# Kernel optimization log

Measured on AMD Instinct MI355X. Metric: run time of the kernel, lower is better.

## Reference

```python
import jax, jax.numpy as jnp
import numpy as np

N_USERS = 100000
N_ITEMS = 50000
D = 64
E = 3200000
N_LAYERS = 2
ALPHA = 0.1


def setup_inputs() -> dict:
    key = jax.random.key(0)
    k1, k2, k3, k4 = jax.random.split(key, 4)
    user_emb0 = jax.random.normal(k1, (N_USERS, D), jnp.float32) * 0.01
    item_emb0 = jax.random.normal(k2, (N_ITEMS, D), jnp.float32) * 0.01
    edge_u = jax.random.randint(k3, (E,), 0, N_USERS, dtype=jnp.int32)
    edge_i = jax.random.randint(k4, (E,), 0, N_ITEMS, dtype=jnp.int32)
    ones = jnp.ones((E,), jnp.float32)
    # row-normalization exactly as the torch module: A_ui = D_u^{-1} R, A_iu = D_i^{-1} R^T
    deg_u = jax.ops.segment_sum(ones, edge_u, num_segments=N_USERS)
    deg_i = jax.ops.segment_sum(ones, edge_i, num_segments=N_ITEMS)
    deg_u = jnp.where(deg_u == 0, 1.0, deg_u)
    deg_i = jnp.where(deg_i == 0, 1.0, deg_i)
    a_ui_vals = 1.0 / deg_u[edge_u]  # value of A_ui at (u, i)
    a_iu_vals = 1.0 / deg_i[edge_i]  # value of A_iu at (i, u)
    return {
        "user_emb0": user_emb0,
        "item_emb0": item_emb0,
        "a_ui_vals": a_ui_vals,
        "a_iu_vals": a_iu_vals,
        "edge_u": edge_u,
        "edge_i": edge_i,
    }


def _spmm(vals, dst_idx, src_idx, src_emb, n_dst):
    # out[dst] = sum_e vals[e] * src_emb[src_idx[e]]  -- gather, scale, scatter-add
    gathered = src_emb[src_idx] * vals[:, None]  # [E, D]
    return jax.ops.segment_sum(gathered, dst_idx, num_segments=n_dst)


def reference(user_emb0, item_emb0, a_ui_vals, a_iu_vals, edge_u, edge_i):
    user_layers = [user_emb0]
    item_layers = [item_emb0]
    for _ in range(N_LAYERS):
        u_new = _spmm(a_ui_vals, edge_u, edge_i, item_layers[-1], N_USERS) + ALPHA * user_emb0
        i_new = _spmm(a_iu_vals, edge_i, edge_u, user_layers[-1], N_ITEMS) + ALPHA * item_emb0
        user_layers.append(u_new)
        item_layers.append(i_new)
    # [n_layers+1, N_USERS, D], [n_layers+1, N_ITEMS, D]
    return jnp.stack(user_layers, 0), jnp.stack(item_layers, 0)
```

## Files before the change

### kernel.cpp

```cpp
#include <hip/hip_runtime.h>


constexpr int N_USERS = 100000;
constexpr int N_ITEMS = 50000;
constexpr int N_ROWS  = N_USERS + N_ITEMS;
constexpr int D = 64;
constexpr int E_EDGES = 3200000;
constexpr float ALPHA = 0.1f;

constexpr long long NUF = (long long)N_USERS * D;
constexpr long long NIF = (long long)N_ITEMS * D;

constexpr int SB_SHIFT = 8;
constexpr int SB_ROWS  = 1 << SB_SHIFT;
constexpr int NSB      = (N_ROWS + SB_ROWS - 1) >> SB_SHIFT;
constexpr int CAP      = 20480;

constexpr int P1_EDGES   = 8192;
constexpr int P1_THREADS = 512;
constexpr int P1_EPT     = P1_EDGES / P1_THREADS;
constexpr int P2_THREADS = 512;

__global__ void init_layer0_sb(const float* __restrict__ uemb,
                               const float* __restrict__ iemb,
                               float* __restrict__ out,
                               int* __restrict__ sbcur) {
    if (blockIdx.x == 0) {
        for (int k = threadIdx.x; k < NSB; k += blockDim.x)
            sbcur[k] = k * CAP;
    }
    long long idx = (long long)blockIdx.x * blockDim.x + threadIdx.x;
    if (idx < NUF) out[idx] = uemb[idx];
    if (idx < NIF) out[3 * NUF + idx] = iemb[idx];
}

__global__ void init_layer0(const float* __restrict__ uemb,
                            const float* __restrict__ iemb,
                            float* __restrict__ out) {
    long long idx = (long long)blockIdx.x * blockDim.x + threadIdx.x;
    if (idx < NUF) out[idx] = uemb[idx];
    if (idx < NIF) out[3 * NUF + idx] = iemb[idx];
}

__global__ void seed_alpha(const float* __restrict__ uemb,
                           const float* __restrict__ iemb,
                           float* __restrict__ out) {
    long long idx = (long long)blockIdx.x * blockDim.x + threadIdx.x;
    if (idx < NUF) {
        float av = ALPHA * uemb[idx];
        out[NUF + idx] = av;
        out[2 * NUF + idx] = av;
    }
    if (idx < NIF) {
        float av = ALPHA * iemb[idx];
        out[3 * NUF + NIF + idx] = av;
        out[3 * NUF + 2 * NIF + idx] = av;
    }
}

__global__ void phase1_binsort(const int* __restrict__ eu, const int* __restrict__ ei,
                               int* __restrict__ sbcur, unsigned* __restrict__ scratch) {
    __shared__ int hist[NSB];
    __shared__ int gbase[NSB];
    int t = threadIdx.x;
    int nchunks = (E_EDGES + P1_EDGES - 1) / P1_EDGES;
    for (int c = blockIdx.x; c < nchunks; c += gridDim.x) {
        int lo = c * P1_EDGES;
        for (int r = t; r < NSB; r += P1_THREADS) hist[r] = 0;
        __syncthreads();
        unsigned sbr[2 * P1_EPT];
        unsigned val[2 * P1_EPT];
#pragma unroll
        for (int k = 0; k < P1_EPT; k++) {
            int e = lo + k * P1_THREADS + t;
            if (e < E_EDGES) {
                int u = __builtin_nontemporal_load(eu + e);
                int i = __builtin_nontemporal_load(ei + e);
                int r0 = u;
                int r1 = N_USERS + i;
                int sb0 = r0 >> SB_SHIFT;
                int sb1 = r1 >> SB_SHIFT;
                int rk0 = atomicAdd(&hist[sb0], 1);
                int rk1 = atomicAdd(&hist[sb1], 1);
                sbr[2 * k]     = ((unsigned)sb0 << 16) | (unsigned)rk0;
                val[2 * k]     = ((unsigned)(r0 & (SB_ROWS - 1)) << 17) | (unsigned)i;
                sbr[2 * k + 1] = ((unsigned)sb1 << 16) | (unsigned)rk1;
                val[2 * k + 1] = ((unsigned)(r1 & (SB_ROWS - 1)) << 17) | (unsigned)u;
            } else {
                sbr[2 * k]     = 0xFFFFFFFFu;
                sbr[2 * k + 1] = 0xFFFFFFFFu;
            }
        }
        __syncthreads();
        for (int r = t; r < NSB; r += P1_THREADS) {
            int cnt = hist[r];
            gbase[r] = cnt ? atomicAdd(&sbcur[r], cnt) : 0;
        }
        __syncthreads();
#pragma unroll
        for (int k = 0; k < 2 * P1_EPT; k++) {
            if (sbr[k] != 0xFFFFFFFFu) {
                int sb = (int)(sbr[k] >> 16);
                int rk = (int)(sbr[k] & 0xFFFFu);
                int p  = gbase[sb] + rk;
                if (p < (sb + 1) * CAP)
                    scratch[p] = val[k];
            }
        }
        __syncthreads();
    }
}

__global__ void phase2_fused(const unsigned* __restrict__ scratch,
                             const int* __restrict__ sbcur,
                             int* __restrict__ row, int* __restrict__ col) {
    __shared__ unsigned buf[CAP];
    __shared__ int hist[SB_ROWS];
    __shared__ int pscan[SB_ROWS];
    __shared__ int psc[P2_THREADS];
    __shared__ int exls[NSB + 1];
    int sb = blockIdx.x;
    int t = threadIdx.x;
    int a = (2 * t < NSB) ? (sbcur[2 * t] - (2 * t) * CAP) : 0;
    int b = (2 * t + 1 < NSB) ? (sbcur[2 * t + 1] - (2 * t + 1) * CAP) : 0;
    psc[t] = a + b;
    __syncthreads();
    for (int off = 1; off < P2_THREADS; off <<= 1) {
        int x = (t >= off) ? psc[t - off] : 0;
        __syncthreads();
        psc[t] += x;
        __syncthreads();
    }
    int base = psc[t] - (a + b);
    if (2 * t < NSB)     exls[2 * t] = base;
    if (2 * t + 1 < NSB) exls[2 * t + 1] = base + a;
    if (t < SB_ROWS) hist[t] = 0;
    __syncthreads();
    int lo = sb * CAP;
    int n  = sbcur[sb] - lo;
    if (n > CAP) n = CAP;
    int out_lo = exls[sb];
    for (int idx = t; idx < n; idx += P2_THREADS)
        atomicAdd(&hist[scratch[lo + idx] >> 17], 1);
    __syncthreads();
    if (t < SB_ROWS) pscan[t] = hist[t];
    __syncthreads();
    for (int off = 1; off < SB_ROWS; off <<= 1) {
        int x = 0;
        if (t < SB_ROWS && t >= off) x = pscan[t - off];
        __syncthreads();
        if (t < SB_ROWS) pscan[t] += x;
        __syncthreads();
    }
    int excl = 0;
    if (t < SB_ROWS) {
        excl = pscan[t] - hist[t];
        int gr = (sb << SB_SHIFT) + t;
        if (gr <= N_ROWS) row[gr] = out_lo + excl;
    }
    __syncthreads();
    if (t < SB_ROWS) hist[t] = excl;
    __syncthreads();
    for (int idx = t; idx < n; idx += P2_THREADS) {
        unsigned e = scratch[lo + idx];
        int p = atomicAdd(&hist[e >> 17], 1);
        buf[p] = e & 0x1FFFFu;
    }
    __syncthreads();
    for (int k = t; k < n; k += P2_THREADS)
        col[out_lo + k] = (int)buf[k];
}

__global__ void emb_to_int8(const float* __restrict__ uemb,
                            const float* __restrict__ iemb,
                            signed char* __restrict__ q0u,
                            signed char* __restrict__ q0i,
                            float* __restrict__ s0u,
                            float* __restrict__ s0i) {
    long long gtid = (long long)blockIdx.x * blockDim.x + threadIdx.x;
    int wave = (int)(gtid >> 6);
    int lane = (int)(gtid & 63);
    if (wave >= N_ROWS) return;
    const float* src; signed char* q; float* s; int r;
    if (wave < N_USERS) { r = wave; src = uemb; q = q0u; s = s0u; }
    else { r = wave - N_USERS; src = iemb; q = q0i; s = s0i; }
    long long li = ((long long)r << 6) + lane;
    float v = src[li];
    float av = fabsf(v);
#pragma unroll
    for (int off = 32; off > 0; off >>= 1)
        av = fmaxf(av, __shfl_xor(av, off));
    float sc = (av > 0.f) ? av / 127.f : 1.f;
    q[li] = (signed char)rintf(v / sc);
    if (lane == 0) s[r] = sc;
}

__device__ __forceinline__ void pull_row_q(const int* __restrict__ row,
                                           const int* __restrict__ col,
                                           const signed char* __restrict__ qsrc,
                                           const float* __restrict__ ssrc,
                                           const float* __restrict__ e0f,
                                           float* __restrict__ dst,
                                           signed char* __restrict__ qdst,
                                           float* __restrict__ sdst,
                                           int comb_row, int local_row, int lane) {
    int start = __builtin_amdgcn_readfirstlane(row[comb_row]);
    int end   = __builtin_amdgcn_readfirstlane(row[comb_row + 1]);
    int len = end - start;
    float scale = (len > 0) ? 1.0f / (float)len : 0.0f;

    float acc0 = 0.f, acc1 = 0.f, acc2 = 0.f, acc3 = 0.f;
    int j = start;
    for (; j + 16 <= end; j += 16) {
        int c[16];
#pragma unroll
        for (int k = 0; k < 16; k++)
            c[k] = __builtin_nontemporal_load(col + j + k);
        float g[16];
#pragma unroll
        for (int k = 0; k < 16; k++) {
            float sc = ssrc[c[k]];
            int   qv = qsrc[((long long)c[k] << 6) + lane];
            g[k] = sc * (float)qv;
        }
#pragma unroll
        for (int k = 0; k < 16; k += 4) {
            acc0 += g[k];
            acc1 += g[k + 1];
            acc2 += g[k + 2];
            acc3 += g[k + 3];
        }
    }
    for (; j + 4 <= end; j += 4) {
        int c0 = __builtin_nontemporal_load(col + j + 0);
        int c1 = __builtin_nontemporal_load(col + j + 1);
        int c2 = __builtin_nontemporal_load(col + j + 2);
        int c3 = __builtin_nontemporal_load(col + j + 3);
        acc0 += ssrc[c0] * (float)qsrc[((long long)c0 << 6) + lane];
        acc1 += ssrc[c1] * (float)qsrc[((long long)c1 << 6) + lane];
        acc2 += ssrc[c2] * (float)qsrc[((long long)c2 << 6) + lane];
        acc3 += ssrc[c3] * (float)qsrc[((long long)c3 << 6) + lane];
    }
    for (; j < end; j++) {
        int c = __builtin_nontemporal_load(col + j);
        acc0 += ssrc[c] * (float)qsrc[((long long)c << 6) + lane];
    }
    long long li = ((long long)local_row << 6) + lane;
    float e0 = e0f[li];
    float res = scale * ((acc0 + acc1) + (acc2 + acc3)) + ALPHA * e0;
    __builtin_nontemporal_store(res, dst + li);
    if (qdst) {
        float av = fabsf(res);
#pragma unroll
        for (int off = 32; off > 0; off >>= 1)
            av = fmaxf(av, __shfl_xor(av, off));
        float sc = (av > 0.f) ? av / 127.f : 1.f;
        qdst[li] = (signed char)rintf(res / sc);
        if (lane == 0) sdst[local_row] = sc;
    }
}

__global__ void spmm_user_q(const int* __restrict__ row, const int* __restrict__ col,
                            const signed char* __restrict__ q_item,
                            const float* __restrict__ s_item,
                            const float* __restrict__ uemb,
                            float* __restrict__ out_user,
                            signed char* __restrict__ q_out,
                            float* __restrict__ s_out) {
    long long gtid = (long long)blockIdx.x * blockDim.x + threadIdx.x;
    int wave = (int)(gtid >> 6);
    int lane = (int)(gtid & 63);
    if (wave >= N_USERS) return;
    pull_row_q(row, col, q_item, s_item, uemb, out_user, q_out, s_out,
               wave, wave, lane);
}

__global__ void spmm_item_q(const int* __restrict__ row, const int* __restrict__ col,
                            const signed char* __restrict__ q_user,
                            const float* __restrict__ s_user,
                            const float* __restrict__ iemb,
                            float* __restrict__ out_item,
                            signed char* __restrict__ q_out,
                            float* __restrict__ s_out) {
    long long gtid = (long long)blockIdx.x * blockDim.x + threadIdx.x;
    int wave = (int)(gtid >> 6);
    int lane = (int)(gtid & 63);
    if (wave >= N_ITEMS) return;
    pull_row_q(row, col, q_user, s_user, iemb, out_item, q_out, s_out,
               N_USERS + wave, wave, lane);
}

__global__ void spmm_pull(const int* __restrict__ row, const int* __restrict__ col,
                          const float* __restrict__ src_user,
                          const float* __restrict__ src_item,
                          const float* __restrict__ uemb, const float* __restrict__ iemb,
                          float* __restrict__ out_user, float* __restrict__ out_item) {
    long long gtid = (long long)blockIdx.x * blockDim.x + threadIdx.x;
    int wave = (int)(gtid >> 6);
    int lane = (int)(gtid & 63);
    if (wave >= N_ROWS) return;
    const float* src; const float* emb0; float* dst; int r;
    if (wave < N_USERS) {
        r = wave; src = src_item; emb0 = uemb; dst = out_user;
    } else {
        r = wave - N_USERS; src = src_user; emb0 = iemb; dst = out_item;
    }
    int start = __builtin_amdgcn_readfirstlane(row[wave]);
    int end   = __builtin_amdgcn_readfirstlane(row[wave + 1]);
    int len = end - start;
    float scale = (len > 0) ? 1.0f / (float)len : 0.0f;
    float acc0 = 0.f, acc1 = 0.f, acc2 = 0.f, acc3 = 0.f;
    int j = start;
    for (; j + 4 <= end; j += 4) {
        int c0 = col[j + 0], c1 = col[j + 1], c2 = col[j + 2], c3 = col[j + 3];
        acc0 += src[((long long)c0 << 6) + lane];
        acc1 += src[((long long)c1 << 6) + lane];
        acc2 += src[((long long)c2 << 6) + lane];
        acc3 += src[((long long)c3 << 6) + lane];
    }
    for (; j < end; j++) {
        int c = col[j];
        acc0 += src[((long long)c << 6) + lane];
    }
    float res = scale * ((acc0 + acc1) + (acc2 + acc3))
              + ALPHA * emb0[((long long)r << 6) + lane];
    dst[((long long)r << 6) + lane] = res;
}

__global__ void spmm_layer_atomic(const float* __restrict__ a_ui,
                                  const float* __restrict__ a_iu,
                                  const int* __restrict__ edge_u,
                                  const int* __restrict__ edge_i,
                                  const float* __restrict__ src_user,
                                  const float* __restrict__ src_item,
                                  float* __restrict__ dst_user,
                                  float* __restrict__ dst_item) {
    long long gtid = (long long)blockIdx.x * blockDim.x + threadIdx.x;
    long long wave = gtid >> 6;
    int lane = (int)(gtid & 63);
    if (wave < (long long)E_EDGES) {
        int e = (int)wave;
        int u = edge_u[e];
        int i = edge_i[e];
        float x = a_ui[e] * src_item[(long long)i * D + lane];
        __hip_atomic_fetch_add(dst_user + (long long)u * D + lane, x,
                               __ATOMIC_RELAXED, __HIP_MEMORY_SCOPE_AGENT);
    } else if (wave < 2LL * E_EDGES) {
        int e = (int)(wave - E_EDGES);
        int u = edge_u[e];
        int i = edge_i[e];
        float x = a_iu[e] * src_user[(long long)u * D + lane];
        __hip_atomic_fetch_add(dst_item + (long long)i * D + lane, x,
                               __ATOMIC_RELAXED, __HIP_MEMORY_SCOPE_AGENT);
    }
}

extern "C" void kernel_launch(void* const* d_in, const int* in_sizes, int n_in,
                              void* d_out, int out_size, void* d_ws, size_t ws_size,
                              hipStream_t stream) {
    const float* uemb   = (const float*)d_in[0];
    const float* iemb   = (const float*)d_in[1];
    const float* a_ui   = (const float*)d_in[2];
    const float* a_iu   = (const float*)d_in[3];
    const int*   edge_u = (const int*)d_in[4];
    const int*   edge_i = (const int*)d_in[5];
    float* out = (float*)d_out;

    float* u1 = out + NUF;
    float* u2 = out + 2 * NUF;
    float* i1 = out + 3 * NUF + NIF;
    float* i2 = out + 3 * NUF + 2 * NIF;

    unsigned* scratch = (unsigned*)u1;

    signed char* q0u = (signed char*)u2;
    signed char* q0i = q0u + NUF;
    float* s0u = (float*)(q0i + NIF);
    float* s0i = s0u + N_USERS;

    size_t base_ints = (size_t)(N_ROWS + 1) + NSB + 2 * (size_t)E_EDGES;
    size_t need_b = base_ints * 4 + 64;
    size_t need_q = need_b + (size_t)(NUF + NIF) + (size_t)N_ROWS * 4;
    bool tier_b = ws_size >= need_b;
    bool tier_q = ws_size >= need_q;

    if (tier_b) {
        int* w = (int*)d_ws;
        int* row   = w;  w += N_ROWS + 1;
        int* sbcur = w;  w += NSB;
        int* col   = w;  w += 2 * E_EDGES;
        signed char* q1u = (signed char*)w;
        signed char* q1i = q1u + NUF;
        float* s1u = (float*)(q1i + NIF);
        float* s1i = s1u + N_USERS;

        {
            const int threads = 256;
            const int blocks = (int)((NUF + threads - 1) / threads);
            init_layer0_sb<<<blocks, threads, 0, stream>>>(uemb, iemb, out, sbcur);
        }
        const int p1_blocks = (E_EDGES + P1_EDGES - 1) / P1_EDGES;
        phase1_binsort<<<p1_blocks, P1_THREADS, 0, stream>>>(edge_u, edge_i,
                                                             sbcur, scratch);
        phase2_fused<<<NSB, P2_THREADS, 0, stream>>>(scratch, sbcur, row, col);

        const int ublocks = (int)(((long long)N_USERS * 64 + 255) / 256);
        const int iblocks = (int)(((long long)N_ITEMS * 64 + 255) / 256);
        if (tier_q) {
            {
                const long long tthreads = (long long)N_ROWS * 64;
                const int blocks = (int)((tthreads + 255) / 256);
                emb_to_int8<<<blocks, 256, 0, stream>>>(uemb, iemb,
                                                        q0u, q0i, s0u, s0i);
            }
            spmm_user_q<<<ublocks, 256, 0, stream>>>(row, col, q0i, s0i, uemb,
                                                     u1, q1u, s1u);
            spmm_item_q<<<iblocks, 256, 0, stream>>>(row, col, q0u, s0u, iemb,
                                                     i1, q1i, s1i);
            spmm_user_q<<<ublocks, 256, 0, stream>>>(row, col, q1i, s1i, uemb,
                                                     u2, nullptr, nullptr);
            spmm_item_q<<<iblocks, 256, 0, stream>>>(row, col, q1u, s1u, iemb,
                                                     i2, nullptr, nullptr);
        } else {
            const long long tthreads = (long long)N_ROWS * 64;
            const int blocks = (int)((tthreads + 255) / 256);
            spmm_pull<<<blocks, 256, 0, stream>>>(row, col, uemb, iemb,
                                                  uemb, iemb, u1, i1);
            spmm_pull<<<blocks, 256, 0, stream>>>(row, col, u1, i1,
                                                  uemb, iemb, u2, i2);
        }
    } else {
        {
            const int threads = 256;
            const int blocks = (int)((NUF + threads - 1) / threads);
            init_layer0<<<blocks, threads, 0, stream>>>(uemb, iemb, out);
            seed_alpha<<<blocks, threads, 0, stream>>>(uemb, iemb, out);
        }
        const int threads = 256;
        const long long total_threads = 2LL * E_EDGES * 64;
        const int blocks = (int)((total_threads + threads - 1) / threads);
        spmm_layer_atomic<<<blocks, threads, 0, stream>>>(a_ui, a_iu, edge_u, edge_i,
                                                          uemb, iemb, u1, i1);
        spmm_layer_atomic<<<blocks, threads, 0, stream>>>(a_ui, a_iu, edge_u, edge_i,
                                                          u1, i1, u2, i2);
    }
}
```

Baseline: 590.0 us.

## Use fp16 item embeddings for user gathers and split superblock scan into kernel

```diff
diff --git a/kernel.cpp b/kernel.cpp
--- a/kernel.cpp
+++ b/kernel.cpp
@@ -20,19 +20,6 @@
 constexpr int P1_THREADS = 512;
 constexpr int P1_EPT     = P1_EDGES / P1_THREADS;
 constexpr int P2_THREADS = 512;
-
-__global__ void init_layer0_sb(const float* __restrict__ uemb,
-                               const float* __restrict__ iemb,
-                               float* __restrict__ out,
-                               int* __restrict__ sbcur) {
-    if (blockIdx.x == 0) {
-        for (int k = threadIdx.x; k < NSB; k += blockDim.x)
-            sbcur[k] = k * CAP;
-    }
-    long long idx = (long long)blockIdx.x * blockDim.x + threadIdx.x;
-    if (idx < NUF) out[idx] = uemb[idx];
-    if (idx < NIF) out[3 * NUF + idx] = iemb[idx];
-}
 
 __global__ void init_layer0(const float* __restrict__ uemb,
                             const float* __restrict__ iemb,
@@ -55,6 +42,29 @@
         float av = ALPHA * iemb[idx];
         out[3 * NUF + NIF + idx] = av;
         out[3 * NUF + 2 * NIF + idx] = av;
+    }
+}
+
+__global__ void init_sbcur(int* __restrict__ sbcur) {
+    int t = blockIdx.x * blockDim.x + threadIdx.x;
+    if (t < NSB) sbcur[t] = t * CAP;
+}
+
+__global__ void count_scan(const int* __restrict__ sbcur, int* __restrict__ sbstart) {
+    __shared__ int sh[1024];
+    int t = threadIdx.x;
+    int v = (t < NSB) ? (sbcur[t] - t * CAP) : 0;
+    sh[t] = v;
+    __syncthreads();
+    for (int off = 1; off < 1024; off <<= 1) {
+        int x = (t >= off) ? sh[t - off] : 0;
+        __syncthreads();
+        sh[t] += x;
+        __syncthreads();
+    }
+    if (t < NSB) {
+        sbstart[t] = sh[t] - v;
+        if (t == NSB - 1) sbstart[NSB] = sh[t];
     }
 }
 
@@ -113,33 +123,19 @@
 
 __global__ void phase2_fused(const unsigned* __restrict__ scratch,
                              const int* __restrict__ sbcur,
+                             const int* __restrict__ sbstart,
                              int* __restrict__ row, int* __restrict__ col) {
     __shared__ unsigned buf[CAP];
     __shared__ int hist[SB_ROWS];
     __shared__ int pscan[SB_ROWS];
-    __shared__ int psc[P2_THREADS];
-    __shared__ int exls[NSB + 1];
     int sb = blockIdx.x;
     int t = threadIdx.x;
-    int a = (2 * t < NSB) ? (sbcur[2 * t] - (2 * t) * CAP) : 0;
-    int b = (2 * t + 1 < NSB) ? (sbcur[2 * t + 1] - (2 * t + 1) * CAP) : 0;
-    psc[t] = a + b;
-    __syncthreads();
-    for (int off = 1; off < P2_THREADS; off <<= 1) {
-        int x = (t >= off) ? psc[t - off] : 0;
-        __syncthreads();
-        psc[t] += x;
-        __syncthreads();
-    }
-    int base = psc[t] - (a + b);
-    if (2 * t < NSB)     exls[2 * t] = base;
-    if (2 * t + 1 < NSB) exls[2 * t + 1] = base + a;
-    if (t < SB_ROWS) hist[t] = 0;
-    __syncthreads();
     int lo = sb * CAP;
     int n  = sbcur[sb] - lo;
     if (n > CAP) n = CAP;
-    int out_lo = exls[sb];
+    int out_lo = sbstart[sb];
+    if (t < SB_ROWS) hist[t] = 0;
+    __syncthreads();
     for (int idx = t; idx < n; idx += P2_THREADS)
         atomicAdd(&hist[scratch[lo + idx] >> 17], 1);
     __syncthreads();
@@ -171,98 +167,34 @@
         col[out_lo + k] = (int)buf[k];
 }
 
-__global__ void emb_to_int8(const float* __restrict__ uemb,
-                            const float* __restrict__ iemb,
-                            signed char* __restrict__ q0u,
-                            signed char* __restrict__ q0i,
-                            float* __restrict__ s0u,
-                            float* __restrict__ s0i) {
+__global__ void emb_convert_mixed(const float* __restrict__ uemb,
+                                  const float* __restrict__ iemb,
+                                  signed char* __restrict__ q0u,
+                                  float* __restrict__ s0u,
+                                  _Float16* __restrict__ h0i) {
     long long gtid = (long long)blockIdx.x * blockDim.x + threadIdx.x;
     int wave = (int)(gtid >> 6);
     int lane = (int)(gtid & 63);
     if (wave >= N_ROWS) return;
-    const float* src; signed char* q; float* s; int r;
-    if (wave < N_USERS) { r = wave; src = uemb; q = q0u; s = s0u; }
-    else { r = wave - N_USERS; src = iemb; q = q0i; s = s0i; }
-    long long li = ((long long)r << 6) + lane;
-    float v = src[li];
-    float av = fabsf(v);
-#pragma unroll
-    for (int off = 32; off > 0; off >>= 1)
-        av = fmaxf(av, __shfl_xor(av, off));
-    float sc = (av > 0.f) ? av / 127.f : 1.f;
-    q[li] = (signed char)rintf(v / sc);
-    if (lane == 0) s[r] = sc;
-}
-
-__device__ __forceinline__ void pull_row_q(const int* __restrict__ row,
-                                           const int* __restrict__ col,
-                                           const signed char* __restrict__ qsrc,
-                                           const float* __restrict__ ssrc,
-                                           const float* __restrict__ e0f,
-                                           float* __restrict__ dst,
-                                           signed char* __restrict__ qdst,
-                                           float* __restrict__ sdst,
-                                           int comb_row, int local_row, int lane) {
-    int start = __builtin_amdgcn_readfirstlane(row[comb_row]);
-    int end   = __builtin_amdgcn_readfirstlane(row[comb_row + 1]);
-    int len = end - start;
-    float scale = (len > 0) ? 1.0f / (float)len : 0.0f;
-
-    float acc0 = 0.f, acc1 = 0.f, acc2 = 0.f, acc3 = 0.f;
-    int j = start;
-    for (; j + 16 <= end; j += 16) {
-        int c[16];
-#pragma unroll
-        for (int k = 0; k < 16; k++)
-            c[k] = __builtin_nontemporal_load(col + j + k);
-        float g[16];
-#pragma unroll
-        for (int k = 0; k < 16; k++) {
-            float sc = ssrc[c[k]];
-            int   qv = qsrc[((long long)c[k] << 6) + lane];
-            g[k] = sc * (float)qv;
-        }
-#pragma unroll
-        for (int k = 0; k < 16; k += 4) {
-            acc0 += g[k];
-            acc1 += g[k + 1];
-            acc2 += g[k + 2];
-            acc3 += g[k + 3];
-        }
-    }
-    for (; j + 4 <= end; j += 4) {
-        int c0 = __builtin_nontemporal_load(col + j + 0);
-        int c1 = __builtin_nontemporal_load(col + j + 1);
-        int c2 = __builtin_nontemporal_load(col + j + 2);
-        int c3 = __builtin_nontemporal_load(col + j + 3);
-        acc0 += ssrc[c0] * (float)qsrc[((long long)c0 << 6) + lane];
-        acc1 += ssrc[c1] * (float)qsrc[((long long)c1 << 6) + lane];
-        acc2 += ssrc[c2] * (float)qsrc[((long long)c2 << 6) + lane];
-        acc3 += ssrc[c3] * (float)qsrc[((long long)c3 << 6) + lane];
-    }
-    for (; j < end; j++) {
-        int c = __builtin_nontemporal_load(col + j);
-        acc0 += ssrc[c] * (float)qsrc[((long long)c << 6) + lane];
-    }
-    long long li = ((long long)local_row << 6) + lane;
-    float e0 = e0f[li];
-    float res = scale * ((acc0 + acc1) + (acc2 + acc3)) + ALPHA * e0;
-    __builtin_nontemporal_store(res, dst + li);
-    if (qdst) {
-        float av = fabsf(res);
+    if (wave < N_USERS) {
+        long long li = ((long long)wave << 6) + lane;
+        float v = uemb[li];
+        float av = fabsf(v);
 #pragma unroll
         for (int off = 32; off > 0; off >>= 1)
             av = fmaxf(av, __shfl_xor(av, off));
         float sc = (av > 0.f) ? av / 127.f : 1.f;
-        qdst[li] = (signed char)rintf(res / sc);
-        if (lane == 0) sdst[local_row] = sc;
-    }
-}
-
-__global__ void spmm_user_q(const int* __restrict__ row, const int* __restrict__ col,
-                            const signed char* __restrict__ q_item,
-                            const float* __restrict__ s_item,
+        q0u[li] = (signed char)rintf(v / sc);
+        if (lane == 0) s0u[wave] = sc;
+    } else {
+        int r = wave - N_USERS;
+        long long li = ((long long)r << 6) + lane;
+        h0i[li] = (_Float16)iemb[li];
+    }
+}
+
+__global__ void spmm_user_h(const int* __restrict__ row, const int* __restrict__ col,
+                            const _Float16* __restrict__ h_item,
                             const float* __restrict__ uemb,
                             float* __restrict__ out_user,
                             signed char* __restrict__ q_out,
@@ -271,8 +203,56 @@
     int wave = (int)(gtid >> 6);
     int lane = (int)(gtid & 63);
     if (wave >= N_USERS) return;
-    pull_row_q(row, col, q_item, s_item, uemb, out_user, q_out, s_out,
-               wave, wave, lane);
+    int start = __builtin_amdgcn_readfirstlane(row[wave]);
+    int end   = __builtin_amdgcn_readfirstlane(row[wave + 1]);
+    int len = end - start;
+    float scale = (len > 0) ? 1.0f / (float)len : 0.0f;
+
+    float acc0 = 0.f, acc1 = 0.f, acc2 = 0.f, acc3 = 0.f;
+    int j = start;
+    for (; j + 16 <= end; j += 16) {
+        int c[16];
+#pragma unroll
+        for (int k = 0; k < 16; k++)
+            c[k] = __builtin_nontemporal_load(col + j + k);
+        float g[16];
+#pragma unroll
+        for (int k = 0; k < 16; k++)
+            g[k] = (float)h_item[((long long)c[k] << 6) + lane];
+#pragma unroll
+        for (int k = 0; k < 16; k += 4) {
+            acc0 += g[k];
+            acc1 += g[k + 1];
+            acc2 += g[k + 2];
+            acc3 += g[k + 3];
+        }
+    }
+    for (; j + 4 <= end; j += 4) {
+        int c0 = __builtin_nontemporal_load(col + j + 0);
+        int c1 = __builtin_nontemporal_load(col + j + 1);
+        int c2 = __builtin_nontemporal_load(col + j + 2);
+        int c3 = __builtin_nontemporal_load(col + j + 3);
+        acc0 += (float)h_item[((long long)c0 << 6) + lane];
+        acc1 += (float)h_item[((long long)c1 << 6) + lane];
+        acc2 += (float)h_item[((long long)c2 << 6) + lane];
+        acc3 += (float)h_item[((long long)c3 << 6) + lane];
+    }
+    for (; j < end; j++) {
+        int c = __builtin_nontemporal_load(col + j);
+        acc0 += (float)h_item[((long long)c << 6) + lane];
+    }
+    long long li = ((long long)wave << 6) + lane;
+    float res = scale * ((acc0 + acc1) + (acc2 + acc3)) + ALPHA * uemb[li];
+    __builtin_nontemporal_store(res, out_user + li);
+    if (q_out) {
+        float av = fabsf(res);
+#pragma unroll
+        for (int off = 32; off > 0; off >>= 1)
+            av = fmaxf(av, __shfl_xor(av, off));
+        float sc = (av > 0.f) ? av / 127.f : 1.f;
+        q_out[li] = (signed char)rintf(res / sc);
+        if (lane == 0) s_out[wave] = sc;
+    }
 }
 
 __global__ void spmm_item_q(const int* __restrict__ row, const int* __restrict__ col,
@@ -280,14 +260,57 @@
                             const float* __restrict__ s_user,
                             const float* __restrict__ iemb,
                             float* __restrict__ out_item,
-                            signed char* __restrict__ q_out,
-                            float* __restrict__ s_out) {
+                            _Float16* __restrict__ h_out) {
     long long gtid = (long long)blockIdx.x * blockDim.x + threadIdx.x;
     int wave = (int)(gtid >> 6);
     int lane = (int)(gtid & 63);
     if (wave >= N_ITEMS) return;
-    pull_row_q(row, col, q_user, s_user, iemb, out_item, q_out, s_out,
-               N_USERS + wave, wave, lane);
+    int crow = N_USERS + wave;
+    int start = __builtin_amdgcn_readfirstlane(row[crow]);
+    int end   = __builtin_amdgcn_readfirstlane(row[crow + 1]);
+    int len = end - start;
+    float scale = (len > 0) ? 1.0f / (float)len : 0.0f;
+
+    float acc0 = 0.f, acc1 = 0.f, acc2 = 0.f, acc3 = 0.f;
+    int j = start;
+    for (; j + 16 <= end; j += 16) {
+        int c[16];
+#pragma unroll
+        for (int k = 0; k < 16; k++)
+            c[k] = __builtin_nontemporal_load(col + j + k);
+        float g[16];
+#pragma unroll
+        for (int k = 0; k < 16; k++) {
+            float sc = s_user[c[k]];
+            int   qv = q_user[((long long)c[k] << 6) + lane];
+            g[k] = sc * (float)qv;
+        }
+#pragma unroll
+        for (int k = 0; k < 16; k += 4) {
+            acc0 += g[k];
+            acc1 += g[k + 1];
+            acc2 += g[k + 2];
+            acc3 += g[k + 3];
+        }
+    }
+    for (; j + 4 <= end; j += 4) {
+        int c0 = __builtin_nontemporal_load(col + j + 0);
+        int c1 = __builtin_nontemporal_load(col + j + 1);
+        int c2 = __builtin_nontemporal_load(col + j + 2);
+        int c3 = __builtin_nontemporal_load(col + j + 3);
+        acc0 += s_user[c0] * (float)q_user[((long long)c0 << 6) + lane];
+        acc1 += s_user[c1] * (float)q_user[((long long)c1 << 6) + lane];
+        acc2 += s_user[c2] * (float)q_user[((long long)c2 << 6) + lane];
+        acc3 += s_user[c3] * (float)q_user[((long long)c3 << 6) + lane];
+    }
+    for (; j < end; j++) {
+        int c = __builtin_nontemporal_load(col + j);
+        acc0 += s_user[c] * (float)q_user[((long long)c << 6) + lane];
+    }
+    long long li = ((long long)wave << 6) + lane;
+    float res = scale * ((acc0 + acc1) + (acc2 + acc3)) + ALPHA * iemb[li];
+    __builtin_nontemporal_store(res, out_item + li);
+    if (h_out) h_out[li] = (_Float16)res;
 }
 
 __global__ void spmm_pull(const int* __restrict__ row, const int* __restrict__ col,
@@ -374,53 +397,57 @@
     unsigned* scratch = (unsigned*)u1;
 
     signed char* q0u = (signed char*)u2;
-    signed char* q0i = q0u + NUF;
-    float* s0u = (float*)(q0i + NIF);
-    float* s0i = s0u + N_USERS;
-
-    size_t base_ints = (size_t)(N_ROWS + 1) + NSB + 2 * (size_t)E_EDGES;
+    float*       s0u = (float*)(q0u + NUF);
+    _Float16*    h0i = (_Float16*)(s0u + N_USERS);
+
+    size_t base_ints = (size_t)(N_ROWS + 1) + NSB + (NSB + 1) + 2 * (size_t)E_EDGES;
     size_t need_b = base_ints * 4 + 64;
-    size_t need_q = need_b + (size_t)(NUF + NIF) + (size_t)N_ROWS * 4;
+    size_t need_m = need_b + (size_t)NIF * 2
+                  + (size_t)NUF
+                  + (size_t)N_USERS * 4;
     bool tier_b = ws_size >= need_b;
-    bool tier_q = ws_size >= need_q;
+    bool tier_m = ws_size >= need_m;
 
     if (tier_b) {
         int* w = (int*)d_ws;
-        int* row   = w;  w += N_ROWS + 1;
-        int* sbcur = w;  w += NSB;
-        int* col   = w;  w += 2 * E_EDGES;
-        signed char* q1u = (signed char*)w;
-        signed char* q1i = q1u + NUF;
-        float* s1u = (float*)(q1i + NIF);
-        float* s1i = s1u + N_USERS;
+        int* row     = w;  w += N_ROWS + 1;
+        int* sbcur   = w;  w += NSB;
+        int* sbstart = w;  w += NSB + 1;
+        int* col     = w;  w += 2 * E_EDGES;
+        _Float16*    h1i = (_Float16*)w;
+        signed char* q1u = (signed char*)(h1i + NIF);
+        float*       s1u = (float*)(q1u + NUF);
 
         {
             const int threads = 256;
             const int blocks = (int)((NUF + threads - 1) / threads);
-            init_layer0_sb<<<blocks, threads, 0, stream>>>(uemb, iemb, out, sbcur);
-        }
+            init_layer0<<<blocks, threads, 0, stream>>>(uemb, iemb, out);
+        }
+        init_sbcur<<<3, 256, 0, stream>>>(sbcur);
         const int p1_blocks = (E_EDGES + P1_EDGES - 1) / P1_EDGES;
         phase1_binsort<<<p1_blocks, P1_THREADS, 0, stream>>>(edge_u, edge_i,
                                                              sbcur, scratch);
-        phase2_fused<<<NSB, P2_THREADS, 0, stream>>>(scratch, sbcur, row, col);
+        count_scan<<<1, 1024, 0, stream>>>(sbcur, sbstart);
+        phase2_fused<<<NSB, P2_THREADS, 0, stream>>>(scratch, sbcur, sbstart,
+                                                     row, col);
 
         const int ublocks = (int)(((long long)N_USERS * 64 + 255) / 256);
         const int iblocks = (int)(((long long)N_ITEMS * 64 + 255) / 256);
-        if (tier_q) {
+        if (tier_m) {
             {
                 const long long tthreads = (long long)N_ROWS * 64;
                 const int blocks = (int)((tthreads + 255) / 256);
-                emb_to_int8<<<blocks, 256, 0, stream>>>(uemb, iemb,
-                                                        q0u, q0i, s0u, s0i);
+                emb_convert_mixed<<<blocks, 256, 0, stream>>>(uemb, iemb,
+                                                              q0u, s0u, h0i);
             }
-            spmm_user_q<<<ublocks, 256, 0, stream>>>(row, col, q0i, s0i, uemb,
+            spmm_user_h<<<ublocks, 256, 0, stream>>>(row, col, h0i, uemb,
                                                      u1, q1u, s1u);
             spmm_item_q<<<iblocks, 256, 0, stream>>>(row, col, q0u, s0u, iemb,
-                                                     i1, q1i, s1i);
-            spmm_user_q<<<ublocks, 256, 0, stream>>>(row, col, q1i, s1i, uemb,
+                                                     i1, h1i);
+            spmm_user_h<<<ublocks, 256, 0, stream>>>(row, col, h1i, uemb,
                                                      u2, nullptr, nullptr);
             spmm_item_q<<<iblocks, 256, 0, stream>>>(row, col, q1u, s1u, iemb,
-                                                     i2, nullptr, nullptr);
+                                                     i2, nullptr);
         } else {
             const long long tthreads = (long long)N_ROWS * 64;
             const int blocks = (int)((tthreads + 255) / 256);
```

Result: faster. 556.9 us (-5.6%).
